# Optimization experiments

Measured on AMD Instinct MI355X. Metric: run time of the kernel, lower is better.

The kernel has to match this reference:

```python
import jax, jax.numpy as jnp
import numpy as np

TAU = 2.0          # config.init_tau
VTH = 1.0          # config.v_threshold
ALPHA = 4.0        # sigmoid surrogate alpha (spikingjelly default)
EPS = 1e-5
NUM_HEADS = 8

@jax.custom_vjp
def spike(x):
    # Heaviside spike with sigmoid surrogate gradient
    return (x >= 0.0).astype(x.dtype)

def _spike_fwd(x):
    return (x >= 0.0).astype(x.dtype), x

def _spike_bwd(x, g):
    s = jax.nn.sigmoid(ALPHA * x)
    return (g * ALPHA * s * (1.0 - s),)

spike.defvjp(_spike_fwd, _spike_bwd)

def lif(x_seq):
    # multi-step LIF, decay_input=False, hard reset to 0, detach_reset=True
    decay = 1.0 - 1.0 / TAU
    def step(v, xt):
        v = v * decay + xt
        s = spike(v - VTH)
        v = v * (1.0 - jax.lax.stop_gradient(s))
        return v, s
    _, s_seq = jax.lax.scan(step, jnp.zeros_like(x_seq[0]), x_seq)
    return s_seq

def bn(x, p):
    # eval-mode BatchNorm1d: p = [gamma, beta, running_mean, running_var]
    g, b, m, v = p[0], p[1], p[2], p[3]
    return (x - m) * (g * jax.lax.rsqrt(v + EPS)) + b

def rotary(x):
    # lucidrains rotary on (B, H, T, D), interleaved pairs
    B, H, T, D = x.shape
    inv = 1.0 / (10000.0 ** (jnp.arange(0, D, 2, dtype=x.dtype) / D))
    f = jnp.arange(T, dtype=x.dtype)[:, None] * inv      # (T, D/2)
    f = jnp.repeat(f, 2, axis=-1)                        # (T, D)
    xr = x.reshape(B, H, T, D // 2, 2)
    rh = jnp.stack([-xr[..., 1], xr[..., 0]], axis=-1).reshape(B, H, T, D)
    return x * jnp.cos(f) + rh * jnp.sin(f)

def ms_ssa_forward(x, attention_mask, ln_g, ln_b, wq, q_bn, wk, k_bn, wv, v_bn, wp, p_bn):
    T, B, N = x.shape
    H = NUM_HEADS
    D = N // H
    scale = np.float32(1.0 / np.sqrt(D))
    # LayerNorm over feature dim (transpose->LN->transpose is LN over last dim)
    mu = jnp.mean(x, -1, keepdims=True)
    var = jnp.var(x, -1, keepdims=True)
    xn = (x - mu) * jax.lax.rsqrt(var + EPS) * ln_g + ln_b
    xs = lif(xn)  # head_lif

    def branch(w, bnp):
        return lif(bn(jnp.einsum('tbn,mn->tbm', xs, w), bnp))

    # Q: Linear+BN+LIF -> rotary -> LIF2 (note raw reshapes, faithful to source)
    q1 = branch(wq, q_bn)                                          # (T,B,N)
    q = rotary(q1.reshape(T, B, H, D).transpose(1, 2, 0, 3))        # (B,H,T,D)
    q = lif(q.reshape(T, B, N)).reshape(B, H, T, D)
    # K: same structure
    k1 = branch(wk, k_bn)
    k = rotary(k1.reshape(T, B, H, D).transpose(1, 2, 0, 3))
    k = lif(k.reshape(T, B, N)).reshape(B, H, T, D)
    # V
    v = branch(wv, v_bn).reshape(T, B, H, D).transpose(1, 2, 0, 3)  # (B,H,T,D)

    # attn_mode == 'v2' with mask
    attn = jnp.einsum('bhtd,bhsd->bhts', q, k)                      # (B,H,T,T)
    attn = jnp.where(attention_mask[:, None, None, :], attn, 0.0)
    y = jnp.einsum('bhts,bhsd->bhtd', attn, v) * scale
    y = lif(y.transpose(2, 0, 1, 3))                                # attn_lif on (T,B,H,D)
    y = y.reshape(T, B, N)
    y = lif(bn(jnp.einsum('tbn,mn->tbm', y, wp), p_bn))             # proj
    return y

def setup_inputs() -> dict:
    key = jax.random.key(0)
    ks = jax.random.split(key, 10)
    T, B, N = 512, 16, 512
    sc = np.float32(1.0 / np.sqrt(N))
    return {
        'x': jax.random.normal(ks[0], (T, B, N), jnp.float32),
        'attention_mask': jnp.ones((B, T), dtype=bool),
        'ln_g': jnp.ones((N,), jnp.float32),
        'ln_b': jnp.zeros((N,), jnp.float32),
        'wq': jax.random.normal(ks[1], (N, N), jnp.float32) * sc,
        'q_bn': jax.random.uniform(ks[2], (4, N), jnp.float32),
        'wk': jax.random.normal(ks[3], (N, N), jnp.float32) * sc,
        'k_bn': jax.random.uniform(ks[4], (4, N), jnp.float32),
        'wv': jax.random.normal(ks[5], (N, N), jnp.float32) * sc,
        'v_bn': jax.random.uniform(ks[6], (4, N), jnp.float32),
        'wp': jax.random.normal(ks[7], (N, N), jnp.float32) * sc,
        'p_bn': jax.random.uniform(ks[8], (4, N), jnp.float32),
    }

def reference(x, attention_mask, ln_g, ln_b, wq, q_bn, wk, k_bn, wv, v_bn, wp, p_bn):
    return ms_ssa_forward(x, attention_mask, ln_g, ln_b, wq, q_bn, wk, k_bn, wv, v_bn, wp, p_bn)
```

## Files before the change

### kernel.cpp

```cpp
#include <hip/hip_runtime.h>
#include <math.h>

#define TT 512
#define BB 16
#define NN 512
#define HH 8
#define DD 64
#define RR 8192
#define LIF_CH 32

typedef int v4i __attribute__((ext_vector_type(4)));

__device__ __forceinline__ double wave_sum_d(double v){
  #pragma unroll
  for (int off = 32; off > 0; off >>= 1) v += __shfl_xor(v, off, 64);
  return v;
}

__global__ __launch_bounds__(256) void ln_kernel(const float* __restrict__ x,
                                                 const float* __restrict__ lng,
                                                 const float* __restrict__ lnb,
                                                 float* __restrict__ out){
  int row  = (blockIdx.x * 256 + threadIdx.x) >> 6;
  int lane = threadIdx.x & 63;
  const float* src = x + (size_t)row * NN;
  int n0 = lane * 4;
  float4 v0 = *(const float4*)(src + n0);
  float4 v1 = *(const float4*)(src + 256 + n0);
  double e[8] = {v0.x, v0.y, v0.z, v0.w, v1.x, v1.y, v1.z, v1.w};
  double s = 0.0;
  #pragma unroll
  for (int i = 0; i < 8; ++i) s += e[i];
  s = wave_sum_d(s);
  double mean = s * (1.0/512.0);
  double ss = 0.0;
  #pragma unroll
  for (int i = 0; i < 8; ++i){ double d = e[i] - mean; ss += d * d; }
  ss = wave_sum_d(ss);
  double inv = 1.0 / sqrt(ss * (1.0/512.0) + 1e-5);
  float4 g0 = *(const float4*)(lng + n0);
  float4 g1 = *(const float4*)(lng + 256 + n0);
  float4 b0 = *(const float4*)(lnb + n0);
  float4 b1 = *(const float4*)(lnb + 256 + n0);
  double gg[8] = {g0.x, g0.y, g0.z, g0.w, g1.x, g1.y, g1.z, g1.w};
  double bb[8] = {b0.x, b0.y, b0.z, b0.w, b1.x, b1.y, b1.z, b1.w};
  float o[8];
  #pragma unroll
  for (int i = 0; i < 8; ++i)
    o[i] = (float)((e[i] - mean) * inv * gg[i] + bb[i]);
  float* dst = out + (size_t)row * NN;
  *(float4*)(dst + n0)       = make_float4(o[0], o[1], o[2], o[3]);
  *(float4*)(dst + 256 + n0) = make_float4(o[4], o[5], o[6], o[7]);
}

__global__ __launch_bounds__(256) void slice_kernel(const float* __restrict__ w0,
                                                    const float* __restrict__ w1,
                                                    const float* __restrict__ w2,
                                                    const float* __restrict__ w3,
                                                    signed char* __restrict__ out){
  int id = blockIdx.x * 256 + threadIdx.x;
  int wi = id >> 18, e = id & 262143;
  const float* w = wi==0 ? w0 : wi==1 ? w1 : wi==2 ? w2 : w3;
  double q = (double)w[e] * 0x1p39;
  long long Qv = (long long)rint(q);
  signed char* dst = out + ((size_t)(wi*5) << 18) + e;
  #pragma unroll
  for (int j = 0; j < 4; ++j){
    signed char bch = (signed char)(Qv & 255);
    dst[(size_t)j << 18] = bch;
    Qv = (Qv - bch) >> 8;
  }
  dst[(size_t)4 << 18] = (signed char)Qv;
}

__global__ __launch_bounds__(256) void rope_table(double* __restrict__ tab){
  int id = blockIdx.x * 256 + threadIdx.x;
  int t = id >> 5, p = id & 31;
  double inv = pow(10000.0, -(double)p / 32.0);
  double f = (double)t * inv;
  double sn, cs; sincos(f, &sn, &cs);
  tab[id*2] = cs; tab[id*2+1] = sn;
}

__global__ __launch_bounds__(256) void gemm_i8(const unsigned char* __restrict__ A,
                                               const signed char* __restrict__ SL,
                                               float* __restrict__ C, int ldc){
  __shared__ signed char Al[64][80];
  __shared__ signed char Bl[5][64][80];
  int tid = threadIdx.x, l = tid & 63, wv = tid >> 6;
  int r0 = blockIdx.x << 6;
  int m0 = blockIdx.y << 6;
  int mat = m0 >> 9, mm0 = m0 & 511;
  const signed char* Bbase = SL + ((size_t)(mat*5) << 18) + (size_t)mm0 * 512;
  v4i zero = {0,0,0,0};
  v4i acc[4][5];
  #pragma unroll
  for (int rf = 0; rf < 4; ++rf)
    #pragma unroll
    for (int j = 0; j < 5; ++j) acc[rf][j] = zero;
  int row = tid >> 2, ch = tid & 3;
  for (int k0 = 0; k0 < 512; k0 += 64){
    __syncthreads();
    *(uint4*)&Al[row][ch*16] = *(const uint4*)(A + (size_t)(r0+row)*512 + k0 + ch*16);
    #pragma unroll
    for (int j = 0; j < 5; ++j)
      *(uint4*)&Bl[j][row][ch*16] =
        *(const uint4*)(Bbase + ((size_t)j << 18) + (size_t)row*512 + k0 + ch*16);
    __syncthreads();
    v4i bf[5];
    #pragma unroll
    for (int j = 0; j < 5; ++j) bf[j] = *(const v4i*)&Bl[j][wv*16 + (l&15)][(l>>4)*16];
    #pragma unroll
    for (int rf = 0; rf < 4; ++rf){
      v4i af = *(const v4i*)&Al[rf*16 + (l&15)][(l>>4)*16];
      #pragma unroll
      for (int j = 0; j < 5; ++j)
        acc[rf][j] = __builtin_amdgcn_mfma_i32_16x16x64_i8(af, bf[j], acc[rf][j], 0, 0, 0);
    }
  }
  int col = m0 + wv*16 + (l&15);
  #pragma unroll
  for (int rf = 0; rf < 4; ++rf)
    #pragma unroll
    for (int i = 0; i < 4; ++i){
      int r = r0 + rf*16 + ((l>>4)<<2) + i;
      double d = (double)acc[rf][4][i];
      d = d*256.0 + (double)acc[rf][3][i];
      d = d*256.0 + (double)acc[rf][2][i];
      d = d*256.0 + (double)acc[rf][1][i];
      d = d*256.0 + (double)acc[rf][0][i];
      C[(size_t)r*ldc + col] = (float)(d * 0x1p-39);
    }
}

__global__ __launch_bounds__(256) void attn_i8(const unsigned char* __restrict__ Q,
                                               const unsigned char* __restrict__ K,
                                               const unsigned char* __restrict__ V,
                                               const int* __restrict__ mask,
                                               float* __restrict__ Y){
  __shared__ signed char Ql[64][80];
  __shared__ signed char Kl[64][80];
  __shared__ signed char Vt[64][80];
  __shared__ signed char Pl[64][80];
  int tid = threadIdx.x, l = tid & 63, wv = tid >> 6;
  int bh = blockIdx.y, b = bh >> 3, h = bh & 7;
  int t0 = blockIdx.x << 6;
  int row = tid >> 2, ch = tid & 3;
  *(uint4*)&Ql[row][ch*16] = *(const uint4*)(Q + ((size_t)(bh*512 + t0 + row))*64 + ch*16);
  __syncthreads();
  v4i qfrag = *(const v4i*)&Ql[wv*16 + (l&15)][(l>>4)*16];
  v4i zero = {0,0,0,0};
  v4i yac[4] = {zero, zero, zero, zero};
  for (int s0 = 0; s0 < 512; s0 += 64){
    __syncthreads();
    {
      *(uint4*)&Kl[row][ch*16] = *(const uint4*)(K + ((size_t)(bh*512 + s0 + row))*64 + ch*16);
      uint4 vvv = *(const uint4*)(V + (size_t)(s0+row)*RR + b*NN + h*DD + ch*16);
      const unsigned char* pb = (const unsigned char*)&vvv;
      #pragma unroll
      for (int j = 0; j < 16; ++j) Vt[ch*16 + j][row] = pb[j];
    }
    __syncthreads();
    #pragma unroll
    for (int sf = 0; sf < 4; ++sf){
      v4i kf = *(const v4i*)&Kl[sf*16 + (l&15)][(l>>4)*16];
      v4i p = __builtin_amdgcn_mfma_i32_16x16x64_i8(qfrag, kf, zero, 0, 0, 0);
      int col = sf*16 + (l&15);
      int mk = mask[b*512 + s0 + col];
      #pragma unroll
      for (int i = 0; i < 4; ++i)
        Pl[wv*16 + ((l>>4)<<2) + i][col] = mk ? (signed char)p[i] : (signed char)0;
    }
    v4i pf = *(const v4i*)&Pl[wv*16 + (l&15)][(l>>4)*16];
    #pragma unroll
    for (int df = 0; df < 4; ++df){
      v4i vf = *(const v4i*)&Vt[df*16 + (l&15)][(l>>4)*16];
      yac[df] = __builtin_amdgcn_mfma_i32_16x16x64_i8(pf, vf, yac[df], 0, 0, 0);
    }
  }
  #pragma unroll
  for (int df = 0; df < 4; ++df)
    #pragma unroll
    for (int i = 0; i < 4; ++i)
      Y[((size_t)(bh*512 + t0 + wv*16 + ((l>>4)<<2) + i))*64 + df*16 + (l&15)] =
        (float)yac[df][i] * 0.125f;
}

__global__ __launch_bounds__(64) void lif_u8(const float* __restrict__ in,
                                             unsigned char* __restrict__ out){
  int r = blockIdx.x * 64 + threadIdx.x;
  float v = 0.0f;
  for (int t0 = 0; t0 < TT; t0 += LIF_CH){
    float xv[LIF_CH];
    #pragma unroll
    for (int i = 0; i < LIF_CH; ++i) xv[i] = in[(size_t)(t0+i)*RR + r];
    #pragma unroll
    for (int i = 0; i < LIF_CH; ++i){
      v = v * 0.5f + xv[i];
      bool sp = (v >= 1.0f);
      out[(size_t)(t0+i)*RR + r] = sp ? 1 : 0;
      v = sp ? 0.0f : v;
    }
  }
}

__global__ __launch_bounds__(64) void lif2_u8(const float* __restrict__ cq,
                                              const float* __restrict__ ck,
                                              unsigned char* __restrict__ oq,
                                              unsigned char* __restrict__ ok){
  int r = blockIdx.x * 64 + threadIdx.x;
  int sel = r >> 13, rr = r & 8191;
  const float* in = sel ? ck : cq;
  unsigned char* out = sel ? ok : oq;
  float v = 0.0f;
  for (int t0 = 0; t0 < TT; t0 += LIF_CH){
    float xv[LIF_CH];
    #pragma unroll
    for (int i = 0; i < LIF_CH; ++i) xv[i] = in[(size_t)(t0+i)*RR + rr];
    #pragma unroll
    for (int i = 0; i < LIF_CH; ++i){
      v = v * 0.5f + xv[i];
      bool sp = (v >= 1.0f);
      out[(size_t)(t0+i)*RR + rr] = sp ? 1 : 0;
      v = sp ? 0.0f : v;
    }
  }
}

__global__ __launch_bounds__(64) void lif_bn3_u8(const float* __restrict__ in,
                                                 const float* __restrict__ qbn,
                                                 const float* __restrict__ kbn,
                                                 const float* __restrict__ vbn,
                                                 unsigned char* __restrict__ oq,
                                                 unsigned char* __restrict__ ok,
                                                 unsigned char* __restrict__ ov){
  int r = blockIdx.x * 64 + threadIdx.x;
  int mat = r >> 13;
  int rb  = r & 8191;
  int b = rb >> 9, n = rb & 511;
  const float* bnp = (mat == 0) ? qbn : (mat == 1) ? kbn : vbn;
  unsigned char* o = ((mat == 0) ? oq : (mat == 1) ? ok : ov) + b*NN + n;
  double g  = bnp[n];
  double be = bnp[NN + n];
  double m  = bnp[2*NN + n];
  double va = bnp[3*NN + n];
  double sc = g / sqrt(va + 1e-5);
  const float* src = in + (size_t)b*1536 + mat*512 + n;
  float v = 0.0f;
  for (int t0 = 0; t0 < TT; t0 += LIF_CH){
    float xv[LIF_CH];
    #pragma unroll
    for (int i = 0; i < LIF_CH; ++i) xv[i] = src[(size_t)(t0+i)*24576];
    #pragma unroll
    for (int i = 0; i < LIF_CH; ++i){
      float y = (float)(((double)xv[i] - m) * sc + be);
      v = v * 0.5f + y;
      bool sp = (v >= 1.0f);
      o[(size_t)(t0+i)*RR] = sp ? 1 : 0;
      v = sp ? 0.0f : v;
    }
  }
}

__global__ __launch_bounds__(64) void lif_bn_f32(const float* __restrict__ in,
                                                 const float* __restrict__ bnp,
                                                 float* __restrict__ out){
  int r = blockIdx.x * 64 + threadIdx.x;
  int n = r & (NN - 1);
  double g  = bnp[n];
  double be = bnp[NN + n];
  double m  = bnp[2*NN + n];
  double va = bnp[3*NN + n];
  double sc = g / sqrt(va + 1e-5);
  float v = 0.0f;
  for (int t0 = 0; t0 < TT; t0 += LIF_CH){
    float xv[LIF_CH];
    #pragma unroll
    for (int i = 0; i < LIF_CH; ++i) xv[i] = in[(size_t)(t0+i)*RR + r];
    #pragma unroll
    for (int i = 0; i < LIF_CH; ++i){
      float y = (float)(((double)xv[i] - m) * sc + be);
      v = v * 0.5f + y;
      bool sp = (v >= 1.0f);
      out[(size_t)(t0+i)*RR + r] = sp ? 1.0f : 0.0f;
      v = sp ? 0.0f : v;
    }
  }
}

__global__ __launch_bounds__(64) void lif_attn_u8(const float* __restrict__ in,
                                                  unsigned char* __restrict__ out){
  int r = blockIdx.x * 64 + threadIdx.x;
  int bh = r >> 6, d = r & 63;
  int b = bh >> 3, h = bh & 7;
  const float* src = in + (size_t)bh * TT * DD + d;
  unsigned char* dst = out + b * NN + h * DD + d;
  float v = 0.0f;
  for (int t0 = 0; t0 < TT; t0 += LIF_CH){
    float xv[LIF_CH];
    #pragma unroll
    for (int i = 0; i < LIF_CH; ++i) xv[i] = src[(size_t)(t0+i)*DD];
    #pragma unroll
    for (int i = 0; i < LIF_CH; ++i){
      v = v * 0.5f + xv[i];
      bool sp = (v >= 1.0f);
      dst[(size_t)(t0+i)*RR] = sp ? 1 : 0;
      v = sp ? 0.0f : v;
    }
  }
}

__global__ __launch_bounds__(256) void rotary2_u8(const unsigned char* __restrict__ q1,
                                                  const unsigned char* __restrict__ k1,
                                                  const double* __restrict__ tab,
                                                  float* __restrict__ oq,
                                                  float* __restrict__ ok){
  int pid = blockIdx.x * 256 + threadIdx.x;
  int sel = pid >> 21;
  int id  = pid & ((1 << 21) - 1);
  int p  = id & 31;
  int t  = (id >> 5) & (TT - 1);
  int bh = id >> 14;
  int b  = bh >> 3, h = bh & 7;
  const unsigned char* s = (sel ? k1 : q1) + ((size_t)(t*BB + b))*NN + h*DD + p*2;
  double x0 = (double)s[0], x1 = (double)s[1];
  double cs = tab[(t*32 + p)*2], sn = tab[(t*32 + p)*2 + 1];
  float2 o;
  o.x = (float)(x0*cs - x1*sn);
  o.y = (float)(x1*cs + x0*sn);
  *(float2*)((sel ? ok : oq) + ((size_t)(bh*TT + t))*DD + p*2) = o;
}

extern "C" void kernel_launch(void* const* d_in, const int* in_sizes, int n_in,
                              void* d_out, int out_size, void* d_ws, size_t ws_size,
                              hipStream_t stream){
  (void)in_sizes; (void)n_in; (void)out_size; (void)ws_size;
  const float* x    = (const float*)d_in[0];
  const int*   mask = (const int*)d_in[1];
  const float* lng  = (const float*)d_in[2];
  const float* lnb  = (const float*)d_in[3];
  const float* wq   = (const float*)d_in[4];
  const float* qbn  = (const float*)d_in[5];
  const float* wk   = (const float*)d_in[6];
  const float* kbn  = (const float*)d_in[7];
  const float* wv   = (const float*)d_in[8];
  const float* vbn  = (const float*)d_in[9];
  const float* wp   = (const float*)d_in[10];
  const float* pbn  = (const float*)d_in[11];
  float* out = (float*)d_out;

  const size_t MB = 1ull << 20;
  char* ws = (char*)d_ws;
  float* C3          = (float*)(ws);
  unsigned char* XS  = (unsigned char*)(ws + 48*MB);
  unsigned char* T1Q = (unsigned char*)(ws + 52*MB);
  unsigned char* T1K = (unsigned char*)(ws + 56*MB);
  unsigned char* Qb  = (unsigned char*)(ws + 60*MB);
  unsigned char* Kb  = (unsigned char*)(ws + 64*MB);
  unsigned char* Vb  = (unsigned char*)(ws + 68*MB);
  signed char*   SLI = (signed char*)(ws + 72*MB);
  double*        TAB = (double*)(ws + 77*MB);
  float* CQ = C3;
  float* CK = C3 + 4*MB;
  float* Y  = C3 + 8*MB;

  rope_table<<<64, 256, 0, stream>>>(TAB);
  slice_kernel<<<4096, 256, 0, stream>>>(wq, wk, wv, wp, SLI);

  ln_kernel<<<2048, 256, 0, stream>>>(x, lng, lnb, C3);
  lif_u8<<<128, 64, 0, stream>>>(C3, XS);

  gemm_i8<<<dim3(128, 24), 256, 0, stream>>>(XS, SLI, C3, 1536);
  lif_bn3_u8<<<384, 64, 0, stream>>>(C3, qbn, kbn, vbn, T1Q, T1K, Vb);
  rotary2_u8<<<16384, 256, 0, stream>>>(T1Q, T1K, TAB, CQ, CK);
  lif2_u8<<<256, 64, 0, stream>>>(CQ, CK, Qb, Kb);

  attn_i8<<<dim3(8, 128), 256, 0, stream>>>(Qb, Kb, Vb, mask, Y);
  lif_attn_u8<<<128, 64, 0, stream>>>(Y, T1Q);

  gemm_i8<<<dim3(128, 8), 256, 0, stream>>>(T1Q, SLI + 15*262144, C3, 512);
  lif_bn_f32<<<128, 64, 0, stream>>>(C3, pbn, out);
}
```

Baseline: 347.1 us.

## Pack operands in MFMA fragment layout, fuse rotary into LIF, double-buffer LIF loads

Weights, spike activations, Q/K/V are now written directly in 16x16 MFMA fragment-tiled layouts, so the GEMM loads contiguous fragments and attention reads K/V fragments straight from global memory without LDS staging or transposes. The GEMM tile grows to 128 rows per block. Rotary and the second LIF are fused into one kernel that exploits binary inputs, using a float4 cos/sin table with precomputed cos±sin. This removes the float intermediates. All LIF kernels double-buffer their time-chunk loads to hide latency. The cost is more complex indexing and less reuse of K/V across waves in attention.

```diff
diff --git a/kernel.cpp b/kernel.cpp
--- a/kernel.cpp
+++ b/kernel.cpp
@@ -7,7 +7,6 @@
 #define HH 8
 #define DD 64
 #define RR 8192
-#define LIF_CH 32
 
 typedef int v4i __attribute__((ext_vector_type(4)));
 
@@ -16,6 +15,7 @@
   for (int off = 32; off > 0; off >>= 1) v += __shfl_xor(v, off, 64);
   return v;
 }
+
 
 __global__ __launch_bounds__(256) void ln_kernel(const float* __restrict__ x,
                                                  const float* __restrict__ lng,
@@ -53,17 +53,19 @@
   *(float4*)(dst + 256 + n0) = make_float4(o[4], o[5], o[6], o[7]);
 }
 
-__global__ __launch_bounds__(256) void slice_kernel(const float* __restrict__ w0,
-                                                    const float* __restrict__ w1,
-                                                    const float* __restrict__ w2,
-                                                    const float* __restrict__ w3,
-                                                    signed char* __restrict__ out){
+__global__ __launch_bounds__(256) void slice_pack(const float* __restrict__ w0,
+                                                  const float* __restrict__ w1,
+                                                  const float* __restrict__ w2,
+                                                  const float* __restrict__ w3,
+                                                  signed char* __restrict__ out){
   int id = blockIdx.x * 256 + threadIdx.x;
   int wi = id >> 18, e = id & 262143;
   const float* w = wi==0 ? w0 : wi==1 ? w1 : wi==2 ? w2 : w3;
   double q = (double)w[e] * 0x1p39;
   long long Qv = (long long)rint(q);
-  signed char* dst = out + ((size_t)(wi*5) << 18) + e;
+  int m = e >> 9, k = e & 511;
+  size_t poff = (size_t)(m >> 4) * 8192 + (size_t)(k >> 4) * 256 + (m & 15) * 16 + (k & 15);
+  signed char* dst = out + ((size_t)(wi*5) << 18) + poff;
   #pragma unroll
   for (int j = 0; j < 4; ++j){
     signed char bch = (signed char)(Qv & 255);
@@ -73,63 +75,71 @@
   dst[(size_t)4 << 18] = (signed char)Qv;
 }
 
-__global__ __launch_bounds__(256) void rope_table(double* __restrict__ tab){
+__global__ __launch_bounds__(256) void rope_tabf(float4* __restrict__ tab){
   int id = blockIdx.x * 256 + threadIdx.x;
   int t = id >> 5, p = id & 31;
   double inv = pow(10000.0, -(double)p / 32.0);
   double f = (double)t * inv;
   double sn, cs; sincos(f, &sn, &cs);
-  tab[id*2] = cs; tab[id*2+1] = sn;
+  tab[id] = make_float4((float)cs, (float)sn, (float)(cs - sn), (float)(cs + sn));
 }
 
 __global__ __launch_bounds__(256) void gemm_i8(const unsigned char* __restrict__ A,
                                                const signed char* __restrict__ SL,
                                                float* __restrict__ C, int ldc){
-  __shared__ signed char Al[64][80];
-  __shared__ signed char Bl[5][64][80];
+  __shared__ __align__(16) unsigned char Ls[28 * 1024];
   int tid = threadIdx.x, l = tid & 63, wv = tid >> 6;
-  int r0 = blockIdx.x << 6;
+  int r0 = blockIdx.x << 7;
   int m0 = blockIdx.y << 6;
   int mat = m0 >> 9, mm0 = m0 & 511;
-  const signed char* Bbase = SL + ((size_t)(mat*5) << 18) + (size_t)mm0 * 512;
+  const unsigned char* Abase = A + (size_t)(r0 >> 4) * 8192 + l * 16;
+  const signed char*  Bbase = SL + ((size_t)(mat*5) << 18) + (size_t)(mm0 >> 4) * 8192 + l * 16;
   v4i zero = {0,0,0,0};
-  v4i acc[4][5];
-  #pragma unroll
-  for (int rf = 0; rf < 4; ++rf)
+  v4i acc[8][5];
+  #pragma unroll
+  for (int rf = 0; rf < 8; ++rf)
     #pragma unroll
     for (int j = 0; j < 5; ++j) acc[rf][j] = zero;
-  int row = tid >> 2, ch = tid & 3;
   for (int k0 = 0; k0 < 512; k0 += 64){
+    int kc = (k0 >> 4) << 8;
     __syncthreads();
-    *(uint4*)&Al[row][ch*16] = *(const uint4*)(A + (size_t)(r0+row)*512 + k0 + ch*16);
-    #pragma unroll
-    for (int j = 0; j < 5; ++j)
-      *(uint4*)&Bl[j][row][ch*16] =
-        *(const uint4*)(Bbase + ((size_t)j << 18) + (size_t)row*512 + k0 + ch*16);
+    #pragma unroll
+    for (int c = 0; c < 7; ++c){
+      int ch = wv + (c << 2);
+      uint4 dat;
+      if (ch < 8){
+        dat = *(const uint4*)(Abase + (size_t)ch * 8192 + kc);
+      } else {
+        int bc = ch - 8; int mg = bc / 5, jj = bc % 5;
+        dat = *(const uint4*)(Bbase + ((size_t)jj << 18) + (size_t)mg * 8192 + kc);
+      }
+      *(uint4*)(Ls + ch * 1024 + l * 16) = dat;
+    }
     __syncthreads();
     v4i bf[5];
     #pragma unroll
-    for (int j = 0; j < 5; ++j) bf[j] = *(const v4i*)&Bl[j][wv*16 + (l&15)][(l>>4)*16];
-    #pragma unroll
-    for (int rf = 0; rf < 4; ++rf){
-      v4i af = *(const v4i*)&Al[rf*16 + (l&15)][(l>>4)*16];
+    for (int j = 0; j < 5; ++j)
+      bf[j] = *(const v4i*)(Ls + 8192 + (wv * 5 + j) * 1024 + l * 16);
+    #pragma unroll
+    for (int rf = 0; rf < 8; ++rf){
+      v4i af = *(const v4i*)(Ls + rf * 1024 + l * 16);
       #pragma unroll
       for (int j = 0; j < 5; ++j)
         acc[rf][j] = __builtin_amdgcn_mfma_i32_16x16x64_i8(af, bf[j], acc[rf][j], 0, 0, 0);
     }
   }
-  int col = m0 + wv*16 + (l&15);
-  #pragma unroll
-  for (int rf = 0; rf < 4; ++rf)
+  int col = m0 + wv * 16 + (l & 15);
+  #pragma unroll
+  for (int rf = 0; rf < 8; ++rf)
     #pragma unroll
     for (int i = 0; i < 4; ++i){
-      int r = r0 + rf*16 + ((l>>4)<<2) + i;
+      int r = r0 + rf * 16 + ((l >> 4) << 2) + i;
       double d = (double)acc[rf][4][i];
       d = d*256.0 + (double)acc[rf][3][i];
       d = d*256.0 + (double)acc[rf][2][i];
       d = d*256.0 + (double)acc[rf][1][i];
       d = d*256.0 + (double)acc[rf][0][i];
-      C[(size_t)r*ldc + col] = (float)(d * 0x1p-39);
+      C[(size_t)r * ldc + col] = (float)(d * 0x1p-39);
     }
 }
 
@@ -138,43 +148,31 @@
                                                const unsigned char* __restrict__ V,
                                                const int* __restrict__ mask,
                                                float* __restrict__ Y){
-  __shared__ signed char Ql[64][80];
-  __shared__ signed char Kl[64][80];
-  __shared__ signed char Vt[64][80];
-  __shared__ signed char Pl[64][80];
+  __shared__ __align__(16) signed char Pl[4096];
   int tid = threadIdx.x, l = tid & 63, wv = tid >> 6;
-  int bh = blockIdx.y, b = bh >> 3, h = bh & 7;
+  int bh = blockIdx.y, b = bh >> 3;
   int t0 = blockIdx.x << 6;
-  int row = tid >> 2, ch = tid & 3;
-  *(uint4*)&Ql[row][ch*16] = *(const uint4*)(Q + ((size_t)(bh*512 + t0 + row))*64 + ch*16);
-  __syncthreads();
-  v4i qfrag = *(const v4i*)&Ql[wv*16 + (l&15)][(l>>4)*16];
+  const unsigned char* Qb = Q + (size_t)bh * 32768;
+  const unsigned char* Kb = K + (size_t)bh * 32768;
+  const unsigned char* Vb = V + (size_t)bh * 32768;
+  v4i qf = *(const v4i*)(Qb + ((size_t)((t0 >> 4) + wv)) * 1024 + l * 16);
   v4i zero = {0,0,0,0};
   v4i yac[4] = {zero, zero, zero, zero};
+  signed char* Pw = Pl + wv * 1024;
   for (int s0 = 0; s0 < 512; s0 += 64){
-    __syncthreads();
-    {
-      *(uint4*)&Kl[row][ch*16] = *(const uint4*)(K + ((size_t)(bh*512 + s0 + row))*64 + ch*16);
-      uint4 vvv = *(const uint4*)(V + (size_t)(s0+row)*RR + b*NN + h*DD + ch*16);
-      const unsigned char* pb = (const unsigned char*)&vvv;
-      #pragma unroll
-      for (int j = 0; j < 16; ++j) Vt[ch*16 + j][row] = pb[j];
-    }
-    __syncthreads();
     #pragma unroll
     for (int sf = 0; sf < 4; ++sf){
-      v4i kf = *(const v4i*)&Kl[sf*16 + (l&15)][(l>>4)*16];
-      v4i p = __builtin_amdgcn_mfma_i32_16x16x64_i8(qfrag, kf, zero, 0, 0, 0);
-      int col = sf*16 + (l&15);
-      int mk = mask[b*512 + s0 + col];
+      v4i kf = *(const v4i*)(Kb + ((size_t)((s0 >> 4) + sf)) * 1024 + l * 16);
+      v4i p = __builtin_amdgcn_mfma_i32_16x16x64_i8(qf, kf, zero, 0, 0, 0);
+      int mk = mask[b * 512 + s0 + sf * 16 + (l & 15)];
       #pragma unroll
       for (int i = 0; i < 4; ++i)
-        Pl[wv*16 + ((l>>4)<<2) + i][col] = mk ? (signed char)p[i] : (signed char)0;
-    }
-    v4i pf = *(const v4i*)&Pl[wv*16 + (l&15)][(l>>4)*16];
+        Pw[sf * 256 + (l >> 4) * 64 + i * 16 + (l & 15)] = mk ? (signed char)p[i] : (signed char)0;
+    }
+    v4i pf = *(const v4i*)(Pw + l * 16);
     #pragma unroll
     for (int df = 0; df < 4; ++df){
-      v4i vf = *(const v4i*)&Vt[df*16 + (l&15)][(l>>4)*16];
+      v4i vf = *(const v4i*)(Vb + (size_t)df * 8192 + ((s0 >> 4)) * 256 + l * 16);
       yac[df] = __builtin_amdgcn_mfma_i32_16x16x64_i8(pf, vf, yac[df], 0, 0, 0);
     }
   }
@@ -182,46 +180,38 @@
   for (int df = 0; df < 4; ++df)
     #pragma unroll
     for (int i = 0; i < 4; ++i)
-      Y[((size_t)(bh*512 + t0 + wv*16 + ((l>>4)<<2) + i))*64 + df*16 + (l&15)] =
+      Y[((size_t)(bh * 512 + t0 + wv * 16 + ((l >> 4) << 2) + i)) * 64 + df * 16 + (l & 15)] =
         (float)yac[df][i] * 0.125f;
 }
 
 __global__ __launch_bounds__(64) void lif_u8(const float* __restrict__ in,
                                              unsigned char* __restrict__ out){
   int r = blockIdx.x * 64 + threadIdx.x;
+  int b = r >> 9, n = r & 511;
+  unsigned char* op = out + (size_t)(n >> 4) * 256 + b * 16 + (n & 15);
+  float xa[32], xb[32];
   float v = 0.0f;
-  for (int t0 = 0; t0 < TT; t0 += LIF_CH){
-    float xv[LIF_CH];
-    #pragma unroll
-    for (int i = 0; i < LIF_CH; ++i) xv[i] = in[(size_t)(t0+i)*RR + r];
-    #pragma unroll
-    for (int i = 0; i < LIF_CH; ++i){
-      v = v * 0.5f + xv[i];
-      bool sp = (v >= 1.0f);
-      out[(size_t)(t0+i)*RR + r] = sp ? 1 : 0;
-      v = sp ? 0.0f : v;
-    }
-  }
-}
-
-__global__ __launch_bounds__(64) void lif2_u8(const float* __restrict__ cq,
-                                              const float* __restrict__ ck,
-                                              unsigned char* __restrict__ oq,
-                                              unsigned char* __restrict__ ok){
-  int r = blockIdx.x * 64 + threadIdx.x;
-  int sel = r >> 13, rr = r & 8191;
-  const float* in = sel ? ck : cq;
-  unsigned char* out = sel ? ok : oq;
-  float v = 0.0f;
-  for (int t0 = 0; t0 < TT; t0 += LIF_CH){
-    float xv[LIF_CH];
-    #pragma unroll
-    for (int i = 0; i < LIF_CH; ++i) xv[i] = in[(size_t)(t0+i)*RR + rr];
-    #pragma unroll
-    for (int i = 0; i < LIF_CH; ++i){
-      v = v * 0.5f + xv[i];
-      bool sp = (v >= 1.0f);
-      out[(size_t)(t0+i)*RR + rr] = sp ? 1 : 0;
+  #pragma unroll
+  for (int i = 0; i < 32; ++i) xa[i] = in[(size_t)i * RR + r];
+  for (int t0 = 0; t0 < TT; t0 += 64){
+    #pragma unroll
+    for (int i = 0; i < 32; ++i) xb[i] = in[(size_t)(t0 + 32 + i) * RR + r];
+    #pragma unroll
+    for (int i = 0; i < 32; ++i){
+      v = v * 0.5f + xa[i];
+      bool sp = (v >= 1.0f);
+      op[(size_t)(t0 + i) * 8192] = sp ? 1 : 0;
+      v = sp ? 0.0f : v;
+    }
+    if (t0 + 64 < TT){
+      #pragma unroll
+      for (int i = 0; i < 32; ++i) xa[i] = in[(size_t)(t0 + 64 + i) * RR + r];
+    }
+    #pragma unroll
+    for (int i = 0; i < 32; ++i){
+      v = v * 0.5f + xb[i];
+      bool sp = (v >= 1.0f);
+      op[(size_t)(t0 + 32 + i) * 8192] = sp ? 1 : 0;
       v = sp ? 0.0f : v;
     }
   }
@@ -239,24 +229,149 @@
   int rb  = r & 8191;
   int b = rb >> 9, n = rb & 511;
   const float* bnp = (mat == 0) ? qbn : (mat == 1) ? kbn : vbn;
-  unsigned char* o = ((mat == 0) ? oq : (mat == 1) ? ok : ov) + b*NN + n;
   double g  = bnp[n];
   double be = bnp[NN + n];
   double m  = bnp[2*NN + n];
   double va = bnp[3*NN + n];
   double sc = g / sqrt(va + 1e-5);
-  const float* src = in + (size_t)b*1536 + mat*512 + n;
+  const float* src = in + (size_t)b * 1536 + mat * 512 + n;
+  bool packed = (mat == 2);
+  int h = n >> 6, d = n & 63;
+  unsigned char* obase;
+  if (packed) obase = ov + (size_t)(b * 8 + h) * 32768 + (size_t)(d >> 4) * 8192 + (d & 15) * 16;
+  else        obase = ((mat == 0) ? oq : ok) + (size_t)b * NN + n;
+  float xa[32], xb[32];
   float v = 0.0f;
-  for (int t0 = 0; t0 < TT; t0 += LIF_CH){
-    float xv[LIF_CH];
-    #pragma unroll
-    for (int i = 0; i < LIF_CH; ++i) xv[i] = src[(size_t)(t0+i)*24576];
-    #pragma unroll
-    for (int i = 0; i < LIF_CH; ++i){
-      float y = (float)(((double)xv[i] - m) * sc + be);
+  #pragma unroll
+  for (int i = 0; i < 32; ++i) xa[i] = src[(size_t)i * 24576];
+  for (int t0 = 0; t0 < TT; t0 += 64){
+    #pragma unroll
+    for (int i = 0; i < 32; ++i) xb[i] = src[(size_t)(t0 + 32 + i) * 24576];
+    #pragma unroll
+    for (int i = 0; i < 32; ++i){
+      int t = t0 + i;
+      float y = (float)(((double)xa[i] - m) * sc + be);
       v = v * 0.5f + y;
       bool sp = (v >= 1.0f);
-      o[(size_t)(t0+i)*RR] = sp ? 1 : 0;
+      size_t off = packed ? ((size_t)(t >> 4) * 256 + (t & 15)) : ((size_t)t * RR);
+      obase[off] = sp ? 1 : 0;
+      v = sp ? 0.0f : v;
+    }
+    if (t0 + 64 < TT){
+      #pragma unroll
+      for (int i = 0; i < 32; ++i) xa[i] = src[(size_t)(t0 + 64 + i) * 24576];
+    }
+    #pragma unroll
+    for (int i = 0; i < 32; ++i){
+      int t = t0 + 32 + i;
+      float y = (float)(((double)xb[i] - m) * sc + be);
+      v = v * 0.5f + y;
+      bool sp = (v >= 1.0f);
+      size_t off = packed ? ((size_t)(t >> 4) * 256 + (t & 15)) : ((size_t)t * RR);
+      obase[off] = sp ? 1 : 0;
+      v = sp ? 0.0f : v;
+    }
+  }
+}
+
+__global__ __launch_bounds__(64) void lif_rot2(const unsigned char* __restrict__ q1,
+                                               const unsigned char* __restrict__ k1,
+                                               const float4* __restrict__ tab,
+                                               unsigned char* __restrict__ oq,
+                                               unsigned char* __restrict__ ok){
+  int j = blockIdx.x * 64 + threadIdx.x;
+  int sel = j >> 13, jr = j & 8191;
+  int t7 = jr >> 6, d = jr & 63, p = d >> 1, odd = d & 1;
+  const unsigned char* in = sel ? k1 : q1;
+  unsigned char* outp = sel ? ok : oq;
+  float4 tv0 = tab[((0 << 7 | t7) << 5) + p];
+  float4 tv1 = tab[((1 << 7 | t7) << 5) + p];
+  float4 tv2 = tab[((2 << 7 | t7) << 5) + p];
+  float4 tv3 = tab[((3 << 7 | t7) << 5) + p];
+  int xa[32], xb[32];
+  float v = 0.0f;
+  #pragma unroll
+  for (int i = 0; i < 32; ++i){
+    int s = i; int bhh = s >> 2, t = ((s & 3) << 7) | t7;
+    xa[i] = in[((size_t)t * 16 + (bhh >> 3)) * 512 + (bhh & 7) * 64 + d];
+  }
+  for (int s0 = 0; s0 < TT; s0 += 64){
+    #pragma unroll
+    for (int i = 0; i < 32; ++i){
+      int s = s0 + 32 + i; int bhh = s >> 2, t = ((s & 3) << 7) | t7;
+      xb[i] = in[((size_t)t * 16 + (bhh >> 3)) * 512 + (bhh & 7) * 64 + d];
+    }
+    #pragma unroll
+    for (int i = 0; i < 32; ++i){
+      int s = s0 + i; int c = s & 3; int bhh = s >> 2;
+      int xs = xa[i];
+      int xp = __shfl_xor(xs, 1, 64);
+      float4 tt = (c == 0) ? tv0 : (c == 1) ? tv1 : (c == 2) ? tv2 : tv3;
+      float val = xs ? (xp ? (odd ? tt.w : tt.z) : tt.x)
+                     : (xp ? (odd ? tt.y : -tt.y) : 0.0f);
+      v = v * 0.5f + val;
+      bool sp = (v >= 1.0f);
+      int t = (c << 7) | t7;
+      outp[(size_t)bhh * 32768 + ((size_t)(t >> 4) * 4 + (d >> 4)) * 256 + (t & 15) * 16 + (d & 15)] = sp ? 1 : 0;
+      v = sp ? 0.0f : v;
+    }
+    if (s0 + 64 < TT){
+      #pragma unroll
+      for (int i = 0; i < 32; ++i){
+        int s = s0 + 64 + i; int bhh = s >> 2, t = ((s & 3) << 7) | t7;
+        xa[i] = in[((size_t)t * 16 + (bhh >> 3)) * 512 + (bhh & 7) * 64 + d];
+      }
+    }
+    #pragma unroll
+    for (int i = 0; i < 32; ++i){
+      int s = s0 + 32 + i; int c = s & 3; int bhh = s >> 2;
+      int xs = xb[i];
+      int xp = __shfl_xor(xs, 1, 64);
+      float4 tt = (c == 0) ? tv0 : (c == 1) ? tv1 : (c == 2) ? tv2 : tv3;
+      float val = xs ? (xp ? (odd ? tt.w : tt.z) : tt.x)
+                     : (xp ? (odd ? tt.y : -tt.y) : 0.0f);
+      v = v * 0.5f + val;
+      bool sp = (v >= 1.0f);
+      int t = (c << 7) | t7;
+      outp[(size_t)bhh * 32768 + ((size_t)(t >> 4) * 4 + (d >> 4)) * 256 + (t & 15) * 16 + (d & 15)] = sp ? 1 : 0;
+      v = sp ? 0.0f : v;
+    }
+  }
+}
+
+__global__ __launch_bounds__(64) void lif_attn_u8(const float* __restrict__ in,
+                                                  unsigned char* __restrict__ out){
+  int r = blockIdx.x * 64 + threadIdx.x;
+  int bh = r >> 6, d = r & 63;
+  int b = bh >> 3, h = bh & 7;
+  int n = h * 64 + d;
+  const float* src = in + (size_t)bh * TT * DD + d;
+  unsigned char* op = out + (size_t)(n >> 4) * 256 + b * 16 + (n & 15);
+  float xa[32], xb[32];
+  float v = 0.0f;
+  #pragma unroll
+  for (int i = 0; i < 32; ++i) xa[i] = src[(size_t)i * DD];
+  for (int t0 = 0; t0 < TT; t0 += 64){
+    #pragma unroll
+    for (int i = 0; i < 32; ++i) xb[i] = src[(size_t)(t0 + 32 + i) * DD];
+    #pragma unroll
+    for (int i = 0; i < 32; ++i){
+      int t = t0 + i;
+      v = v * 0.5f + xa[i];
+      bool sp = (v >= 1.0f);
+      op[(size_t)t * 8192] = sp ? 1 : 0;
+      v = sp ? 0.0f : v;
+    }
+    if (t0 + 64 < TT){
+      #pragma unroll
+      for (int i = 0; i < 32; ++i) xa[i] = src[(size_t)(t0 + 64 + i) * DD];
+    }
+    #pragma unroll
+    for (int i = 0; i < 32; ++i){
+      int t = t0 + 32 + i;
+      v = v * 0.5f + xb[i];
+      bool sp = (v >= 1.0f);
+      op[(size_t)t * 8192] = sp ? 1 : 0;
       v = sp ? 0.0f : v;
     }
   }
@@ -272,63 +387,34 @@
   double m  = bnp[2*NN + n];
   double va = bnp[3*NN + n];
   double sc = g / sqrt(va + 1e-5);
+  float xa[32], xb[32];
   float v = 0.0f;
-  for (int t0 = 0; t0 < TT; t0 += LIF_CH){
-    float xv[LIF_CH];
-    #pragma unroll
-    for (int i = 0; i < LIF_CH; ++i) xv[i] = in[(size_t)(t0+i)*RR + r];
-    #pragma unroll
-    for (int i = 0; i < LIF_CH; ++i){
-      float y = (float)(((double)xv[i] - m) * sc + be);
+  #pragma unroll
+  for (int i = 0; i < 32; ++i) xa[i] = in[(size_t)i * RR + r];
+  for (int t0 = 0; t0 < TT; t0 += 64){
+    #pragma unroll
+    for (int i = 0; i < 32; ++i) xb[i] = in[(size_t)(t0 + 32 + i) * RR + r];
+    #pragma unroll
+    for (int i = 0; i < 32; ++i){
+      float y = (float)(((double)xa[i] - m) * sc + be);
       v = v * 0.5f + y;
       bool sp = (v >= 1.0f);
-      out[(size_t)(t0+i)*RR + r] = sp ? 1.0f : 0.0f;
-      v = sp ? 0.0f : v;
-    }
-  }
-}
-
-__global__ __launch_bounds__(64) void lif_attn_u8(const float* __restrict__ in,
-                                                  unsigned char* __restrict__ out){
-  int r = blockIdx.x * 64 + threadIdx.x;
-  int bh = r >> 6, d = r & 63;
-  int b = bh >> 3, h = bh & 7;
-  const float* src = in + (size_t)bh * TT * DD + d;
-  unsigned char* dst = out + b * NN + h * DD + d;
-  float v = 0.0f;
-  for (int t0 = 0; t0 < TT; t0 += LIF_CH){
-    float xv[LIF_CH];
-    #pragma unroll
-    for (int i = 0; i < LIF_CH; ++i) xv[i] = src[(size_t)(t0+i)*DD];
-    #pragma unroll
-    for (int i = 0; i < LIF_CH; ++i){
-      v = v * 0.5f + xv[i];
-      bool sp = (v >= 1.0f);
-      dst[(size_t)(t0+i)*RR] = sp ? 1 : 0;
-      v = sp ? 0.0f : v;
-    }
-  }
-}
-
-__global__ __launch_bounds__(256) void rotary2_u8(const unsigned char* __restrict__ q1,
-                                                  const unsigned char* __restrict__ k1,
-                                                  const double* __restrict__ tab,
-                                                  float* __restrict__ oq,
-                                                  float* __restrict__ ok){
-  int pid = blockIdx.x * 256 + threadIdx.x;
-  int sel = pid >> 21;
-  int id  = pid & ((1 << 21) - 1);
-  int p  = id & 31;
-  int t  = (id >> 5) & (TT - 1);
-  int bh = id >> 14;
-  int b  = bh >> 3, h = bh & 7;
-  const unsigned char* s = (sel ? k1 : q1) + ((size_t)(t*BB + b))*NN + h*DD + p*2;
-  double x0 = (double)s[0], x1 = (double)s[1];
-  double cs = tab[(t*32 + p)*2], sn = tab[(t*32 + p)*2 + 1];
-  float2 o;
-  o.x = (float)(x0*cs - x1*sn);
-  o.y = (float)(x1*cs + x0*sn);
-  *(float2*)((sel ? ok : oq) + ((size_t)(bh*TT + t))*DD + p*2) = o;
+      out[(size_t)(t0 + i) * RR + r] = sp ? 1.0f : 0.0f;
+      v = sp ? 0.0f : v;
+    }
+    if (t0 + 64 < TT){
+      #pragma unroll
+      for (int i = 0; i < 32; ++i) xa[i] = in[(size_t)(t0 + 64 + i) * RR + r];
+    }
+    #pragma unroll
+    for (int i = 0; i < 32; ++i){
+      float y = (float)(((double)xb[i] - m) * sc + be);
+      v = v * 0.5f + y;
+      bool sp = (v >= 1.0f);
+      out[(size_t)(t0 + 32 + i) * RR + r] = sp ? 1.0f : 0.0f;
+      v = sp ? 0.0f : v;
+    }
+  }
 }
 
 extern "C" void kernel_launch(void* const* d_in, const int* in_sizes, int n_in,
@@ -359,25 +445,23 @@
   unsigned char* Kb  = (unsigned char*)(ws + 64*MB);
   unsigned char* Vb  = (unsigned char*)(ws + 68*MB);
   signed char*   SLI = (signed char*)(ws + 72*MB);
-  double*        TAB = (double*)(ws + 77*MB);
-  float* CQ = C3;
-  float* CK = C3 + 4*MB;
-  float* Y  = C3 + 8*MB;
-
-  rope_table<<<64, 256, 0, stream>>>(TAB);
-  slice_kernel<<<4096, 256, 0, stream>>>(wq, wk, wv, wp, SLI);
+  float4*        TABF= (float4*)(ws + 77*MB);
+  float* Y  = C3;
+  float* CP = C3 + 4*MB;
+
+  rope_tabf<<<64, 256, 0, stream>>>(TABF);
+  slice_pack<<<4096, 256, 0, stream>>>(wq, wk, wv, wp, SLI);
 
   ln_kernel<<<2048, 256, 0, stream>>>(x, lng, lnb, C3);
   lif_u8<<<128, 64, 0, stream>>>(C3, XS);
 
-  gemm_i8<<<dim3(128, 24), 256, 0, stream>>>(XS, SLI, C3, 1536);
+  gemm_i8<<<dim3(64, 24), 256, 0, stream>>>(XS, SLI, C3, 1536);
   lif_bn3_u8<<<384, 64, 0, stream>>>(C3, qbn, kbn, vbn, T1Q, T1K, Vb);
-  rotary2_u8<<<16384, 256, 0, stream>>>(T1Q, T1K, TAB, CQ, CK);
-  lif2_u8<<<256, 64, 0, stream>>>(CQ, CK, Qb, Kb);
+  lif_rot2<<<256, 64, 0, stream>>>(T1Q, T1K, TABF, Qb, Kb);
 
   attn_i8<<<dim3(8, 128), 256, 0, stream>>>(Qb, Kb, Vb, mask, Y);
   lif_attn_u8<<<128, 64, 0, stream>>>(Y, T1Q);
 
-  gemm_i8<<<dim3(128, 8), 256, 0, stream>>>(T1Q, SLI + 15*262144, C3, 512);
-  lif_bn_f32<<<128, 64, 0, stream>>>(C3, pbn, out);
-}
+  gemm_i8<<<dim3(64, 8), 256, 0, stream>>>(T1Q, SLI + ((size_t)15 << 18), CP, 512);
+  lif_bn_f32<<<128, 64, 0, stream>>>(CP, pbn, out);
+}
```

After: 325.5 us. 6.2% less time.
